# Performance work log

Measured on AMD Instinct MI355X. Metric: run time of the kernel, lower is better.

Reference implementation:

```python
import jax, jax.numpy as jnp
import numpy as np
import math

HIDDEN = 1024
HEADS = 16
D_K = HIDDEN // HEADS
B, S = 2, 2048


def setup_inputs() -> dict:
    key = jax.random.key(0)
    ks = jax.random.split(key, 12)
    sc = 1.0 / math.sqrt(HIDDEN)
    inp = {
        "q": jax.random.normal(ks[0], (B, S, HIDDEN), jnp.float32),
        "k": jax.random.normal(ks[1], (B, S, HIDDEN), jnp.float32),
        "v": jax.random.normal(ks[2], (B, S, HIDDEN), jnp.float32),
        "mask": jax.random.randint(ks[3], (B, 1, S, S), 0, 2, jnp.int32),
        "Wq": jax.random.normal(ks[4], (HIDDEN, HIDDEN), jnp.float32) * sc,
        "bq": jnp.zeros((HIDDEN,), jnp.float32),
        "Wk": jax.random.normal(ks[5], (HIDDEN, HIDDEN), jnp.float32) * sc,
        "bk": jnp.zeros((HIDDEN,), jnp.float32),
        "Wv": jax.random.normal(ks[6], (HIDDEN, HIDDEN), jnp.float32) * sc,
        "bv": jnp.zeros((HIDDEN,), jnp.float32),
        "Wo": jax.random.normal(ks[7], (HIDDEN, HIDDEN), jnp.float32) * sc,
        "bo": jnp.zeros((HIDDEN,), jnp.float32),
    }
    return inp


def reference(q, k, v, mask, Wq, bq, Wk, bk, Wv, bv, Wo, bo):
    bs, sq, _ = q.shape
    # project and split heads: [b, h, s, d_k]
    qh = (q @ Wq + bq).reshape(bs, sq, HEADS, D_K).transpose(0, 2, 1, 3)
    kh = (k @ Wk + bk).reshape(bs, -1, HEADS, D_K).transpose(0, 2, 1, 3)
    vh = (v @ Wv + bv).reshape(bs, -1, HEADS, D_K).transpose(0, 2, 1, 3)
    scores = jnp.einsum("bhqd,bhkd->bhqk", qh, kh) / math.sqrt(D_K)
    scores = jnp.where(mask == 0, -jnp.inf, scores)
    attn = jax.nn.softmax(scores, axis=-1)
    attn = jnp.nan_to_num(attn, nan=0.0)  # dropout is identity in eval
    x = jnp.einsum("bhqk,bhkd->bhqd", attn, vh)
    x = x.transpose(0, 2, 1, 3).reshape(bs, sq, HIDDEN)
    return x @ Wo + bo
```

## Files before the change

kernel.cpp:

```cpp
#include <hip/hip_runtime.h>
#include <hip/hip_bf16.h>
#include <math.h>

#define HIDDEN 1024
#define HEADS 16
#define DK 64
#define BATCH 2
#define SLEN 2048

typedef __attribute__((ext_vector_type(8))) short short8v;
typedef __attribute__((ext_vector_type(4))) float f32x4;

__device__ __forceinline__ unsigned short bf_hi(float x) {
  unsigned u = __builtin_bit_cast(unsigned, x);
  unsigned r = u + 0x7fffu + ((u >> 16) & 1u);
  return (unsigned short)(r >> 16);
}
__device__ __forceinline__ float bf_f(unsigned short h) {
  unsigned u = ((unsigned)h) << 16;
  return __builtin_bit_cast(float, u);
}
__device__ __forceinline__ unsigned pack_hl(float x) {
  unsigned short hi = bf_hi(x);
  unsigned short lo = bf_hi(x - bf_f(hi));
  return (unsigned)hi | ((unsigned)lo << 16);
}

__device__ __forceinline__ short8v unpack8(const uint4& a0, const uint4& a1,
                                           unsigned sel) {
  uint4 r;
  r.x = __builtin_amdgcn_perm(a0.y, a0.x, sel);
  r.y = __builtin_amdgcn_perm(a0.w, a0.z, sel);
  r.z = __builtin_amdgcn_perm(a1.y, a1.x, sel);
  r.w = __builtin_amdgcn_perm(a1.w, a1.z, sel);
  return __builtin_bit_cast(short8v, r);
}
#define SEL_HI 0x05040100u
#define SEL_LO 0x07060302u

#define GLB_US(p) ((const __attribute__((address_space(1))) unsigned short*)(p))
#define LDS_US(p) ((__attribute__((address_space(3))) unsigned short*)(p))

__global__ __launch_bounds__(256) void mask_bits_kernel(
    const int* __restrict__ mask, unsigned long long* __restrict__ Mb)
{
  const int row = blockIdx.x * 4 + (threadIdx.x >> 6);
  const int lane = threadIdx.x & 63;
  const int* mr = mask + (size_t)row * SLEN;
#pragma unroll
  for (int t = 0; t < 32; ++t) {
    int m = mr[t * 64 + lane];
    unsigned long long bits = __ballot(m != 0);
    if (lane == 0) Mb[(size_t)row * 32 + t] = bits;
  }
}

__global__ __launch_bounds__(256) void pack_act_kernel(
    const float* __restrict__ src, unsigned short* __restrict__ hi,
    unsigned short* __restrict__ lo, int n4)
{
  int stride = gridDim.x * blockDim.x;
  for (int i = blockIdx.x * blockDim.x + threadIdx.x; i < n4; i += stride) {
    float4 v = ((const float4*)src)[i];
    ushort4 H, L;
    H.x = bf_hi(v.x); L.x = bf_hi(v.x - bf_f(H.x));
    H.y = bf_hi(v.y); L.y = bf_hi(v.y - bf_f(H.y));
    H.z = bf_hi(v.z); L.z = bf_hi(v.z - bf_f(H.z));
    H.w = bf_hi(v.w); L.w = bf_hi(v.w - bf_f(H.w));
    *(ushort4*)(hi + (size_t)i * 4) = H;
    *(ushort4*)(lo + (size_t)i * 4) = L;
  }
}

__global__ __launch_bounds__(256) void pack_wT_kernel(
    const float* __restrict__ W, unsigned short* __restrict__ Whi,
    unsigned short* __restrict__ Wlo)
{
  __shared__ float T[64][65];
  const int t = threadIdx.x;
  const int bk = blockIdx.x >> 4, bn = blockIdx.x & 15;
#pragma unroll
  for (int i = 0; i < 4; ++i) {
    int k = (t >> 4) + i * 16, n = (t & 15) * 4;
    float4 v = *(const float4*)(W + (size_t)(bk * 64 + k) * HIDDEN + bn * 64 + n);
    T[k][n + 0] = v.x; T[k][n + 1] = v.y; T[k][n + 2] = v.z; T[k][n + 3] = v.w;
  }
  __syncthreads();
  const int nl = t & 63, kc = (t >> 6) * 16;
#pragma unroll
  for (int i = 0; i < 4; ++i) {
    ushort4 H, L;
    float x0 = T[kc + i * 4 + 0][nl], x1 = T[kc + i * 4 + 1][nl];
    float x2 = T[kc + i * 4 + 2][nl], x3 = T[kc + i * 4 + 3][nl];
    H.x = bf_hi(x0); L.x = bf_hi(x0 - bf_f(H.x));
    H.y = bf_hi(x1); L.y = bf_hi(x1 - bf_f(H.y));
    H.z = bf_hi(x2); L.z = bf_hi(x2 - bf_f(H.z));
    H.w = bf_hi(x3); L.w = bf_hi(x3 - bf_f(H.w));
    size_t base = (size_t)(bn * 64 + nl) * HIDDEN + bk * 64 + kc + i * 4;
    *(ushort4*)(Whi + base) = H;
    *(ushort4*)(Wlo + base) = L;
  }
}

__global__ __launch_bounds__(256) void gemm_sp_kernel(
    const unsigned short* __restrict__ Ahi, const unsigned short* __restrict__ Alo,
    const unsigned short* __restrict__ Bthi, const unsigned short* __restrict__ Btlo,
    const float* __restrict__ bias, unsigned short* __restrict__ Yhi,
    unsigned short* __restrict__ Ylo, float* __restrict__ Yf, int mode)
{
  __shared__ __align__(16) unsigned short Ah[64 * 32], Al_[64 * 32];
  __shared__ __align__(16) unsigned short Bh[64 * 32], Bl[64 * 32];

  const int tid = threadIdx.x;
  const int lb = (blockIdx.x & 7) * 128 + (blockIdx.x >> 3);
  const int bm = lb >> 4, bn = lb & 15;
  const int m0 = bm * 64, n0 = bn * 64;
  const int w = tid >> 6, lane = tid & 63;
  const int wm = w >> 1, wn = w & 1;
  const int g = lane >> 4, qi = lane & 15;

  const int tr = tid >> 2;
  const int tc = (((tid & 3) ^ ((tr >> 2) & 3)) << 3);
  const int dofs = tid * 8;

  f32x4 acc[2][2];
#pragma unroll
  for (int mt = 0; mt < 2; ++mt)
#pragma unroll
    for (int nt = 0; nt < 2; ++nt) acc[mt][nt] = (f32x4){0.f, 0.f, 0.f, 0.f};

  for (int k0 = 0; k0 < HIDDEN; k0 += 32) {
    __syncthreads();
    size_t ga = (size_t)(m0 + tr) * HIDDEN + k0 + tc;
    size_t gb = (size_t)(n0 + tr) * HIDDEN + k0 + tc;
    __builtin_amdgcn_global_load_lds(GLB_US(Ahi + ga), LDS_US(Ah + dofs), 16, 0, 0);
    __builtin_amdgcn_global_load_lds(GLB_US(Alo + ga), LDS_US(Al_ + dofs), 16, 0, 0);
    __builtin_amdgcn_global_load_lds(GLB_US(Bthi + gb), LDS_US(Bh + dofs), 16, 0, 0);
    __builtin_amdgcn_global_load_lds(GLB_US(Btlo + gb), LDS_US(Bl + dofs), 16, 0, 0);
    __syncthreads();

    short8v a_h[2], a_l[2], b_h[2], b_l[2];
#pragma unroll
    for (int mt = 0; mt < 2; ++mt) {
      int R = wm * 32 + mt * 16 + qi;
      int cofs = R * 32 + ((g ^ ((R >> 2) & 3)) << 3);
      a_h[mt] = *(const short8v*)&Ah[cofs];
      a_l[mt] = *(const short8v*)&Al_[cofs];
    }
#pragma unroll
    for (int nt = 0; nt < 2; ++nt) {
      int R = wn * 32 + nt * 16 + qi;
      int cofs = R * 32 + ((g ^ ((R >> 2) & 3)) << 3);
      b_h[nt] = *(const short8v*)&Bh[cofs];
      b_l[nt] = *(const short8v*)&Bl[cofs];
    }
#pragma unroll
    for (int nt = 0; nt < 2; ++nt)
#pragma unroll
      for (int mt = 0; mt < 2; ++mt) {
        acc[mt][nt] = __builtin_amdgcn_mfma_f32_16x16x32_bf16(a_h[mt], b_h[nt], acc[mt][nt], 0, 0, 0);
        acc[mt][nt] = __builtin_amdgcn_mfma_f32_16x16x32_bf16(a_l[mt], b_h[nt], acc[mt][nt], 0, 0, 0);
        acc[mt][nt] = __builtin_amdgcn_mfma_f32_16x16x32_bf16(a_h[mt], b_l[nt], acc[mt][nt], 0, 0, 0);
      }
  }

#pragma unroll
  for (int nt = 0; nt < 2; ++nt) {
    int n = n0 + wn * 32 + nt * 16 + qi;
    float bv = bias[n];
#pragma unroll
    for (int mt = 0; mt < 2; ++mt) {
#pragma unroll
      for (int r = 0; r < 4; ++r) {
        int m = m0 + wm * 32 + mt * 16 + g * 4 + r;
        float val = acc[mt][nt][r] + bv;
        if (mode == 0) {
          Yf[(size_t)m * HIDDEN + n] = val;
        } else {
          int s = m & (SLEN - 1);
          int bh_ = (m >> 11) * HEADS + (n >> 6);
          int d = n & 63;
          unsigned short hi = bf_hi(val);
          unsigned short lo = bf_hi(val - bf_f(hi));
          size_t base = (mode == 1) ? (((size_t)bh_ * SLEN + s) << 6) + d
                                    : ((size_t)(bh_ * DK + d)) * SLEN + s;
          Yhi[base] = hi;
          Ylo[base] = lo;
        }
      }
    }
  }
}

__global__ __launch_bounds__(256) void attn_mfma_kernel(
    const unsigned short* __restrict__ Qhi, const unsigned short* __restrict__ Qlo,
    const unsigned short* __restrict__ Khi, const unsigned short* __restrict__ Klo,
    const unsigned short* __restrict__ Vthi, const unsigned short* __restrict__ Vtlo,
    const unsigned long long* __restrict__ Mb,
    unsigned short* __restrict__ XaHi, unsigned short* __restrict__ XaLo)
{
  __shared__ __align__(16) unsigned char smem[32768];
  unsigned short* Ks_hi = (unsigned short*)smem;
  unsigned short* Ks_lo = (unsigned short*)(smem + 8192);
  unsigned short* Vs_hi = (unsigned short*)(smem + 16384);
  unsigned short* Vs_lo = (unsigned short*)(smem + 24576);

  const int tid = threadIdx.x;
  const int bx = blockIdx.x;
  const int lb = (bx & 7) * 128 + (bx >> 3);
  const int qt = lb & 31;
  const int bh = lb >> 5;
  const int b = bh >> 4, h = bh & 15;
  const int w = tid >> 6, lane = tid & 63;
  const int g = lane >> 4, qi = lane & 15;
  const int qbase = qt * 64 + w * 16;

  unsigned* Pw = (unsigned*)(smem + w * 4096);

  short8v qh[2], ql[2];
  {
    const unsigned short* qr_hi = Qhi + ((size_t)bh * SLEN + qbase + qi) * DK;
    const unsigned short* qr_lo = Qlo + ((size_t)bh * SLEN + qbase + qi) * DK;
    qh[0] = *(const short8v*)(qr_hi + g * 8);
    qh[1] = *(const short8v*)(qr_hi + 32 + g * 8);
    ql[0] = *(const short8v*)(qr_lo + g * 8);
    ql[1] = *(const short8v*)(qr_lo + 32 + g * 8);
  }

  f32x4 o[4];
#pragma unroll
  for (int dt = 0; dt < 4; ++dt) o[dt] = (f32x4){0.f, 0.f, 0.f, 0.f};
  float m_run = -1e30f, l_run = 0.f;

  const unsigned long long* mrow = Mb + ((size_t)b * SLEN + qbase + qi) * 32;

  for (int k0 = 0; k0 < SLEN; k0 += 64) {
    __syncthreads();
#pragma unroll
    for (int i = 0; i < 2; ++i) {
      int rloc = w * 16 + i * 8 + (lane >> 3);
      int col = ((lane & 7) * 8) ^ ((rloc & 7) << 3);
      size_t gk = ((size_t)bh * SLEN + k0 + rloc) * 64 + col;
      size_t gv = ((size_t)(bh * 64 + rloc)) * SLEN + k0 + col;
      int dofs = rloc * 64 + (lane & 7) * 8;
      __builtin_amdgcn_global_load_lds(GLB_US(Khi + gk), LDS_US(Ks_hi + dofs), 16, 0, 0);
      __builtin_amdgcn_global_load_lds(GLB_US(Klo + gk), LDS_US(Ks_lo + dofs), 16, 0, 0);
      __builtin_amdgcn_global_load_lds(GLB_US(Vthi + gv), LDS_US(Vs_hi + dofs), 16, 0, 0);
      __builtin_amdgcn_global_load_lds(GLB_US(Vtlo + gv), LDS_US(Vs_lo + dofs), 16, 0, 0);
    }
    __syncthreads();

    f32x4 sf[4];
#pragma unroll
    for (int ks = 0; ks < 4; ++ks) {
      int krow = ks * 16 + qi;
      int cswz = (krow & 7) << 3;
      short8v kh0 = *(const short8v*)&Ks_hi[krow * 64 + ((g * 8) ^ cswz)];
      short8v kh1 = *(const short8v*)&Ks_hi[krow * 64 + ((32 + g * 8) ^ cswz)];
      short8v kl0 = *(const short8v*)&Ks_lo[krow * 64 + ((g * 8) ^ cswz)];
      short8v kl1 = *(const short8v*)&Ks_lo[krow * 64 + ((32 + g * 8) ^ cswz)];
      f32x4 s = {0.f, 0.f, 0.f, 0.f};
      s = __builtin_amdgcn_mfma_f32_16x16x32_bf16(kh0, qh[0], s, 0, 0, 0);
      s = __builtin_amdgcn_mfma_f32_16x16x32_bf16(kh1, qh[1], s, 0, 0, 0);
      s = __builtin_amdgcn_mfma_f32_16x16x32_bf16(kh0, ql[0], s, 0, 0, 0);
      s = __builtin_amdgcn_mfma_f32_16x16x32_bf16(kh1, ql[1], s, 0, 0, 0);
      s = __builtin_amdgcn_mfma_f32_16x16x32_bf16(kl0, qh[0], s, 0, 0, 0);
      s = __builtin_amdgcn_mfma_f32_16x16x32_bf16(kl1, qh[1], s, 0, 0, 0);
      sf[ks] = s;
    }
    __syncthreads();

    unsigned long long mw = mrow[k0 >> 6];
    unsigned s0 = ((unsigned)mw) >> (g * 4);
    unsigned s1 = ((unsigned)(mw >> 32)) >> (g * 4);
    float sv[4][4];
    float rowmax = -INFINITY;
#pragma unroll
    for (int ks = 0; ks < 4; ++ks) {
      unsigned sel = (ks < 2) ? s0 : s1;
#pragma unroll
      for (int r = 0; r < 4; ++r) {
        float x = sf[ks][r] * 0.125f;
        sv[ks][r] = ((sel >> (((ks & 1) << 4) + r)) & 1) ? x : -INFINITY;
        rowmax = fmaxf(rowmax, sv[ks][r]);
      }
    }
    rowmax = fmaxf(rowmax, __shfl_xor(rowmax, 16));
    rowmax = fmaxf(rowmax, __shfl_xor(rowmax, 32));

    if (__any(rowmax > m_run + 8.f)) {
      float mnew = fmaxf(m_run, rowmax);
      float scale = __expf(m_run - mnew);
      l_run *= scale;
#pragma unroll
      for (int r = 0; r < 4; ++r) {
        float sc = __shfl(scale, g * 4 + r);
        o[0][r] *= sc; o[1][r] *= sc; o[2][r] *= sc; o[3][r] *= sc;
      }
      m_run = mnew;
    }

    float lsum = 0.f;
#pragma unroll
    for (int ks = 0; ks < 4; ++ks)
#pragma unroll
      for (int r = 0; r < 4; ++r) {
        float pv = __expf(sv[ks][r] - m_run);
        lsum += pv;
        int k = ks * 16 + g * 4 + r;
        int wa = (k << 4) + qi;
        wa ^= ((wa >> 7) & 1) << 4;
        Pw[wa] = pack_hl(pv);
      }
    lsum += __shfl_xor(lsum, 16);
    lsum += __shfl_xor(lsum, 32);
    l_run += lsum;

#pragma unroll
    for (int kh = 0; kh < 2; ++kh) {
      unsigned u0, u1, u2, u3, u4, u5, u6, u7;
      {
        int kb = kh * 32 + g * 8;
        int ra;
        ra = ((kb + 0) << 4) + qi; ra ^= ((ra >> 7) & 1) << 4; u0 = Pw[ra];
        ra = ((kb + 1) << 4) + qi; ra ^= ((ra >> 7) & 1) << 4; u1 = Pw[ra];
        ra = ((kb + 2) << 4) + qi; ra ^= ((ra >> 7) & 1) << 4; u2 = Pw[ra];
        ra = ((kb + 3) << 4) + qi; ra ^= ((ra >> 7) & 1) << 4; u3 = Pw[ra];
        ra = ((kb + 4) << 4) + qi; ra ^= ((ra >> 7) & 1) << 4; u4 = Pw[ra];
        ra = ((kb + 5) << 4) + qi; ra ^= ((ra >> 7) & 1) << 4; u5 = Pw[ra];
        ra = ((kb + 6) << 4) + qi; ra ^= ((ra >> 7) & 1) << 4; u6 = Pw[ra];
        ra = ((kb + 7) << 4) + qi; ra ^= ((ra >> 7) & 1) << 4; u7 = Pw[ra];
      }
      uint4 a0 = {u0, u1, u2, u3}, a1 = {u4, u5, u6, u7};
      short8v phi = unpack8(a0, a1, SEL_HI);
      short8v plo = unpack8(a0, a1, SEL_LO);
#pragma unroll
      for (int dt = 0; dt < 4; ++dt) {
        int drow = dt * 16 + qi;
        int vcol = (kh * 32 + g * 8) ^ ((drow & 7) << 3);
        short8v vh = *(const short8v*)&Vs_hi[drow * 64 + vcol];
        short8v vl = *(const short8v*)&Vs_lo[drow * 64 + vcol];
        o[dt] = __builtin_amdgcn_mfma_f32_16x16x32_bf16(phi, vh, o[dt], 0, 0, 0);
        o[dt] = __builtin_amdgcn_mfma_f32_16x16x32_bf16(phi, vl, o[dt], 0, 0, 0);
        o[dt] = __builtin_amdgcn_mfma_f32_16x16x32_bf16(plo, vh, o[dt], 0, 0, 0);
      }
    }
  }

#pragma unroll
  for (int r = 0; r < 4; ++r) {
    float lr = __shfl(l_run, g * 4 + r);
    float inv = lr > 0.f ? 1.f / lr : 0.f;
    size_t rowa = ((size_t)(b * SLEN) + qbase + g * 4 + r) * HIDDEN + h * DK;
#pragma unroll
    for (int dt = 0; dt < 4; ++dt) {
      float val = o[dt][r] * inv;
      unsigned short hi = bf_hi(val);
      XaHi[rowa + dt * 16 + qi] = hi;
      XaLo[rowa + dt * 16 + qi] = bf_hi(val - bf_f(hi));
    }
  }
}

extern "C" void kernel_launch(void* const* d_in, const int* in_sizes, int n_in,
                              void* d_out, int out_size, void* d_ws, size_t ws_size,
                              hipStream_t stream) {
  const float* q   = (const float*)d_in[0];
  const float* k   = (const float*)d_in[1];
  const float* v   = (const float*)d_in[2];
  const int*  mask = (const int*)d_in[3];
  const float* Wq  = (const float*)d_in[4];
  const float* bq  = (const float*)d_in[5];
  const float* Wk  = (const float*)d_in[6];
  const float* bk  = (const float*)d_in[7];
  const float* Wv  = (const float*)d_in[8];
  const float* bv  = (const float*)d_in[9];
  const float* Wo  = (const float*)d_in[10];
  const float* bo  = (const float*)d_in[11];
  float* out = (float*)d_out;

  const size_t HSZ = (size_t)BATCH * SLEN * HIDDEN;
  const size_t WSZ = (size_t)HIDDEN * HIDDEN;
  unsigned short* wsu = (unsigned short*)d_ws;
  unsigned short* Qhi = wsu;
  unsigned short* Qlo = wsu + HSZ;
  unsigned short* Khi = wsu + 2 * HSZ;
  unsigned short* Klo = wsu + 3 * HSZ;
  unsigned short* Vthi = wsu + 4 * HSZ;
  unsigned short* Vtlo = wsu + 5 * HSZ;
  unsigned short* Ahi_ = wsu + 6 * HSZ;
  unsigned short* Alo_ = wsu + 7 * HSZ;
  unsigned short* Wthi = wsu + 8 * HSZ;
  unsigned short* Wtlo = wsu + 8 * HSZ + WSZ;
  unsigned long long* Mb = (unsigned long long*)(wsu + 8 * HSZ + 2 * WSZ);

  const int n4 = (int)(HSZ / 4);

  mask_bits_kernel<<<BATCH * SLEN / 4, 256, 0, stream>>>(mask, Mb);

  pack_act_kernel<<<1024, 256, 0, stream>>>(q, Ahi_, Alo_, n4);
  pack_wT_kernel<<<256, 256, 0, stream>>>(Wq, Wthi, Wtlo);
  gemm_sp_kernel<<<1024, 256, 0, stream>>>(Ahi_, Alo_, Wthi, Wtlo, bq, Qhi, Qlo, nullptr, 1);
  pack_act_kernel<<<1024, 256, 0, stream>>>(k, Ahi_, Alo_, n4);
  pack_wT_kernel<<<256, 256, 0, stream>>>(Wk, Wthi, Wtlo);
  gemm_sp_kernel<<<1024, 256, 0, stream>>>(Ahi_, Alo_, Wthi, Wtlo, bk, Khi, Klo, nullptr, 1);
  pack_act_kernel<<<1024, 256, 0, stream>>>(v, Ahi_, Alo_, n4);
  pack_wT_kernel<<<256, 256, 0, stream>>>(Wv, Wthi, Wtlo);
  gemm_sp_kernel<<<1024, 256, 0, stream>>>(Ahi_, Alo_, Wthi, Wtlo, bv, Vthi, Vtlo, nullptr, 2);

  attn_mfma_kernel<<<1024, 256, 0, stream>>>(Qhi, Qlo, Khi, Klo, Vthi, Vtlo,
                                             Mb, Ahi_, Alo_);

  pack_wT_kernel<<<256, 256, 0, stream>>>(Wo, Wthi, Wtlo);
  gemm_sp_kernel<<<1024, 256, 0, stream>>>(Ahi_, Alo_, Wthi, Wtlo, bo, nullptr, nullptr, out, 0);
}
```

Before: 507.2 us.

## Double-buffer GEMM LDS loads, fold softmax scale into Q, use exp2 and truncating split

The split-bf16 projection GEMM now uses two LDS buffers, so the next K-slice's global-to-LDS load is issued before computing on the current one, with one barrier per iteration instead of two. The block-to-tile mapping is changed to group M tiles per XCD. The 1/sqrt(d)*log2(e) factor is folded into the Q projection epilogue so attention can use exp2f without a per-score multiply, and the rescale threshold is adjusted to match. The hi/lo bf16 split now truncates instead of rounding, which is cheaper but leaves a slightly larger residual in the low part.

```diff
diff --git a/kernel.cpp b/kernel.cpp
--- a/kernel.cpp
+++ b/kernel.cpp
@@ -11,19 +11,22 @@
 typedef __attribute__((ext_vector_type(8))) short short8v;
 typedef __attribute__((ext_vector_type(4))) float f32x4;
 
-__device__ __forceinline__ unsigned short bf_hi(float x) {
-  unsigned u = __builtin_bit_cast(unsigned, x);
-  unsigned r = u + 0x7fffu + ((u >> 16) & 1u);
-  return (unsigned short)(r >> 16);
-}
 __device__ __forceinline__ float bf_f(unsigned short h) {
   unsigned u = ((unsigned)h) << 16;
   return __builtin_bit_cast(float, u);
 }
-__device__ __forceinline__ unsigned pack_hl(float x) {
-  unsigned short hi = bf_hi(x);
-  unsigned short lo = bf_hi(x - bf_f(hi));
-  return (unsigned)hi | ((unsigned)lo << 16);
+__device__ __forceinline__ void split_t(float x, unsigned short& hi,
+                                        unsigned short& lo) {
+  unsigned xu = __builtin_bit_cast(unsigned, x);
+  float r = x - __builtin_bit_cast(float, xu & 0xffff0000u);
+  hi = (unsigned short)(xu >> 16);
+  lo = (unsigned short)(__builtin_bit_cast(unsigned, r) >> 16);
+}
+__device__ __forceinline__ unsigned pack_hl_t(float x) {
+  unsigned xu = __builtin_bit_cast(unsigned, x);
+  float r = x - __builtin_bit_cast(float, xu & 0xffff0000u);
+  unsigned ru = __builtin_bit_cast(unsigned, r);
+  return __builtin_amdgcn_perm(ru, xu, 0x07060302u);
 }
 
 __device__ __forceinline__ short8v unpack8(const uint4& a0, const uint4& a1,
@@ -41,6 +44,8 @@
 #define GLB_US(p) ((const __attribute__((address_space(1))) unsigned short*)(p))
 #define LDS_US(p) ((__attribute__((address_space(3))) unsigned short*)(p))
 
+#define QSCALE 0.18033688011112042f
+
 __global__ __launch_bounds__(256) void mask_bits_kernel(
     const int* __restrict__ mask, unsigned long long* __restrict__ Mb)
 {
@@ -63,10 +68,8 @@
   for (int i = blockIdx.x * blockDim.x + threadIdx.x; i < n4; i += stride) {
     float4 v = ((const float4*)src)[i];
     ushort4 H, L;
-    H.x = bf_hi(v.x); L.x = bf_hi(v.x - bf_f(H.x));
-    H.y = bf_hi(v.y); L.y = bf_hi(v.y - bf_f(H.y));
-    H.z = bf_hi(v.z); L.z = bf_hi(v.z - bf_f(H.z));
-    H.w = bf_hi(v.w); L.w = bf_hi(v.w - bf_f(H.w));
+    split_t(v.x, H.x, L.x); split_t(v.y, H.y, L.y);
+    split_t(v.z, H.z, L.z); split_t(v.w, H.w, L.w);
     *(ushort4*)(hi + (size_t)i * 4) = H;
     *(ushort4*)(lo + (size_t)i * 4) = L;
   }
@@ -90,12 +93,10 @@
 #pragma unroll
   for (int i = 0; i < 4; ++i) {
     ushort4 H, L;
-    float x0 = T[kc + i * 4 + 0][nl], x1 = T[kc + i * 4 + 1][nl];
-    float x2 = T[kc + i * 4 + 2][nl], x3 = T[kc + i * 4 + 3][nl];
-    H.x = bf_hi(x0); L.x = bf_hi(x0 - bf_f(H.x));
-    H.y = bf_hi(x1); L.y = bf_hi(x1 - bf_f(H.y));
-    H.z = bf_hi(x2); L.z = bf_hi(x2 - bf_f(H.z));
-    H.w = bf_hi(x3); L.w = bf_hi(x3 - bf_f(H.w));
+    split_t(T[kc + i * 4 + 0][nl], H.x, L.x);
+    split_t(T[kc + i * 4 + 1][nl], H.y, L.y);
+    split_t(T[kc + i * 4 + 2][nl], H.z, L.z);
+    split_t(T[kc + i * 4 + 3][nl], H.w, L.w);
     size_t base = (size_t)(bn * 64 + nl) * HIDDEN + bk * 64 + kc + i * 4;
     *(ushort4*)(Whi + base) = H;
     *(ushort4*)(Wlo + base) = L;
@@ -105,15 +106,17 @@
 __global__ __launch_bounds__(256) void gemm_sp_kernel(
     const unsigned short* __restrict__ Ahi, const unsigned short* __restrict__ Alo,
     const unsigned short* __restrict__ Bthi, const unsigned short* __restrict__ Btlo,
-    const float* __restrict__ bias, unsigned short* __restrict__ Yhi,
-    unsigned short* __restrict__ Ylo, float* __restrict__ Yf, int mode)
+    const float* __restrict__ bias, float oscale,
+    unsigned short* __restrict__ Yhi, unsigned short* __restrict__ Ylo,
+    float* __restrict__ Yf, int mode)
 {
-  __shared__ __align__(16) unsigned short Ah[64 * 32], Al_[64 * 32];
-  __shared__ __align__(16) unsigned short Bh[64 * 32], Bl[64 * 32];
+  __shared__ __align__(16) unsigned short lds[2][4][64 * 32];
 
   const int tid = threadIdx.x;
-  const int lb = (blockIdx.x & 7) * 128 + (blockIdx.x >> 3);
-  const int bm = lb >> 4, bn = lb & 15;
+  const int xcd = blockIdx.x & 7;
+  const int idx = blockIdx.x >> 3;
+  const int bm = xcd * 8 + (idx & 7);
+  const int bn = idx >> 3;
   const int m0 = bm * 64, n0 = bn * 64;
   const int w = tid >> 6, lane = tid & 63;
   const int wm = w >> 1, wn = w & 1;
@@ -129,30 +132,30 @@
 #pragma unroll
     for (int nt = 0; nt < 2; ++nt) acc[mt][nt] = (f32x4){0.f, 0.f, 0.f, 0.f};
 
-  for (int k0 = 0; k0 < HIDDEN; k0 += 32) {
-    __syncthreads();
+  auto stage = [&](int buf, int k0) {
     size_t ga = (size_t)(m0 + tr) * HIDDEN + k0 + tc;
     size_t gb = (size_t)(n0 + tr) * HIDDEN + k0 + tc;
-    __builtin_amdgcn_global_load_lds(GLB_US(Ahi + ga), LDS_US(Ah + dofs), 16, 0, 0);
-    __builtin_amdgcn_global_load_lds(GLB_US(Alo + ga), LDS_US(Al_ + dofs), 16, 0, 0);
-    __builtin_amdgcn_global_load_lds(GLB_US(Bthi + gb), LDS_US(Bh + dofs), 16, 0, 0);
-    __builtin_amdgcn_global_load_lds(GLB_US(Btlo + gb), LDS_US(Bl + dofs), 16, 0, 0);
-    __syncthreads();
-
+    __builtin_amdgcn_global_load_lds(GLB_US(Ahi + ga), LDS_US(&lds[buf][0][dofs]), 16, 0, 0);
+    __builtin_amdgcn_global_load_lds(GLB_US(Alo + ga), LDS_US(&lds[buf][1][dofs]), 16, 0, 0);
+    __builtin_amdgcn_global_load_lds(GLB_US(Bthi + gb), LDS_US(&lds[buf][2][dofs]), 16, 0, 0);
+    __builtin_amdgcn_global_load_lds(GLB_US(Btlo + gb), LDS_US(&lds[buf][3][dofs]), 16, 0, 0);
+  };
+
+  auto compute = [&](int buf) {
     short8v a_h[2], a_l[2], b_h[2], b_l[2];
 #pragma unroll
     for (int mt = 0; mt < 2; ++mt) {
       int R = wm * 32 + mt * 16 + qi;
       int cofs = R * 32 + ((g ^ ((R >> 2) & 3)) << 3);
-      a_h[mt] = *(const short8v*)&Ah[cofs];
-      a_l[mt] = *(const short8v*)&Al_[cofs];
+      a_h[mt] = *(const short8v*)&lds[buf][0][cofs];
+      a_l[mt] = *(const short8v*)&lds[buf][1][cofs];
     }
 #pragma unroll
     for (int nt = 0; nt < 2; ++nt) {
       int R = wn * 32 + nt * 16 + qi;
       int cofs = R * 32 + ((g ^ ((R >> 2) & 3)) << 3);
-      b_h[nt] = *(const short8v*)&Bh[cofs];
-      b_l[nt] = *(const short8v*)&Bl[cofs];
+      b_h[nt] = *(const short8v*)&lds[buf][2][cofs];
+      b_l[nt] = *(const short8v*)&lds[buf][3][cofs];
     }
 #pragma unroll
     for (int nt = 0; nt < 2; ++nt)
@@ -162,7 +165,16 @@
         acc[mt][nt] = __builtin_amdgcn_mfma_f32_16x16x32_bf16(a_l[mt], b_h[nt], acc[mt][nt], 0, 0, 0);
         acc[mt][nt] = __builtin_amdgcn_mfma_f32_16x16x32_bf16(a_h[mt], b_l[nt], acc[mt][nt], 0, 0, 0);
       }
-  }
+  };
+
+  stage(0, 0);
+  __syncthreads();
+  for (int t = 0; t < 31; ++t) {
+    stage((t + 1) & 1, (t + 1) * 32);
+    compute(t & 1);
+    __syncthreads();
+  }
+  compute(1);
 
 #pragma unroll
   for (int nt = 0; nt < 2; ++nt) {
@@ -173,15 +185,15 @@
 #pragma unroll
       for (int r = 0; r < 4; ++r) {
         int m = m0 + wm * 32 + mt * 16 + g * 4 + r;
-        float val = acc[mt][nt][r] + bv;
+        float val = (acc[mt][nt][r] + bv) * oscale;
         if (mode == 0) {
           Yf[(size_t)m * HIDDEN + n] = val;
         } else {
           int s = m & (SLEN - 1);
           int bh_ = (m >> 11) * HEADS + (n >> 6);
           int d = n & 63;
-          unsigned short hi = bf_hi(val);
-          unsigned short lo = bf_hi(val - bf_f(hi));
+          unsigned short hi, lo;
+          split_t(val, hi, lo);
           size_t base = (mode == 1) ? (((size_t)bh_ * SLEN + s) << 6) + d
                                     : ((size_t)(bh_ * DK + d)) * SLEN + s;
           Yhi[base] = hi;
@@ -280,7 +292,7 @@
       unsigned sel = (ks < 2) ? s0 : s1;
 #pragma unroll
       for (int r = 0; r < 4; ++r) {
-        float x = sf[ks][r] * 0.125f;
+        float x = sf[ks][r];
         sv[ks][r] = ((sel >> (((ks & 1) << 4) + r)) & 1) ? x : -INFINITY;
         rowmax = fmaxf(rowmax, sv[ks][r]);
       }
@@ -288,9 +300,9 @@
     rowmax = fmaxf(rowmax, __shfl_xor(rowmax, 16));
     rowmax = fmaxf(rowmax, __shfl_xor(rowmax, 32));
 
-    if (__any(rowmax > m_run + 8.f)) {
+    if (__any(rowmax > m_run + 11.5f)) {
       float mnew = fmaxf(m_run, rowmax);
-      float scale = __expf(m_run - mnew);
+      float scale = exp2f(m_run - mnew);
       l_run *= scale;
 #pragma unroll
       for (int r = 0; r < 4; ++r) {
@@ -305,12 +317,12 @@
     for (int ks = 0; ks < 4; ++ks)
 #pragma unroll
       for (int r = 0; r < 4; ++r) {
-        float pv = __expf(sv[ks][r] - m_run);
+        float pv = exp2f(sv[ks][r] - m_run);
         lsum += pv;
         int k = ks * 16 + g * 4 + r;
         int wa = (k << 4) + qi;
         wa ^= ((wa >> 7) & 1) << 4;
-        Pw[wa] = pack_hl(pv);
+        Pw[wa] = pack_hl_t(pv);
       }
     lsum += __shfl_xor(lsum, 16);
     lsum += __shfl_xor(lsum, 32);
@@ -355,9 +367,10 @@
 #pragma unroll
     for (int dt = 0; dt < 4; ++dt) {
       float val = o[dt][r] * inv;
-      unsigned short hi = bf_hi(val);
+      unsigned short hi, lo;
+      split_t(val, hi, lo);
       XaHi[rowa + dt * 16 + qi] = hi;
-      XaLo[rowa + dt * 16 + qi] = bf_hi(val - bf_f(hi));
+      XaLo[rowa + dt * 16 + qi] = lo;
     }
   }
 }
@@ -400,17 +413,17 @@
 
   pack_act_kernel<<<1024, 256, 0, stream>>>(q, Ahi_, Alo_, n4);
   pack_wT_kernel<<<256, 256, 0, stream>>>(Wq, Wthi, Wtlo);
-  gemm_sp_kernel<<<1024, 256, 0, stream>>>(Ahi_, Alo_, Wthi, Wtlo, bq, Qhi, Qlo, nullptr, 1);
+  gemm_sp_kernel<<<1024, 256, 0, stream>>>(Ahi_, Alo_, Wthi, Wtlo, bq, QSCALE, Qhi, Qlo, nullptr, 1);
   pack_act_kernel<<<1024, 256, 0, stream>>>(k, Ahi_, Alo_, n4);
   pack_wT_kernel<<<256, 256, 0, stream>>>(Wk, Wthi, Wtlo);
-  gemm_sp_kernel<<<1024, 256, 0, stream>>>(Ahi_, Alo_, Wthi, Wtlo, bk, Khi, Klo, nullptr, 1);
+  gemm_sp_kernel<<<1024, 256, 0, stream>>>(Ahi_, Alo_, Wthi, Wtlo, bk, 1.0f, Khi, Klo, nullptr, 1);
   pack_act_kernel<<<1024, 256, 0, stream>>>(v, Ahi_, Alo_, n4);
   pack_wT_kernel<<<256, 256, 0, stream>>>(Wv, Wthi, Wtlo);
-  gemm_sp_kernel<<<1024, 256, 0, stream>>>(Ahi_, Alo_, Wthi, Wtlo, bv, Vthi, Vtlo, nullptr, 2);
+  gemm_sp_kernel<<<1024, 256, 0, stream>>>(Ahi_, Alo_, Wthi, Wtlo, bv, 1.0f, Vthi, Vtlo, nullptr, 2);
 
   attn_mfma_kernel<<<1024, 256, 0, stream>>>(Qhi, Qlo, Khi, Klo, Vthi, Vtlo,
                                              Mb, Ahi_, Alo_);
 
   pack_wT_kernel<<<256, 256, 0, stream>>>(Wo, Wthi, Wtlo);
-  gemm_sp_kernel<<<1024, 256, 0, stream>>>(Ahi_, Alo_, Wthi, Wtlo, bo, nullptr, nullptr, out, 0);
-}
+  gemm_sp_kernel<<<1024, 256, 0, stream>>>(Ahi_, Alo_, Wthi, Wtlo, bo, 1.0f, nullptr, nullptr, out, 0);
+}
```

Result: no change. 511.5 us (+0.8%).
